# Performance work log

Measured on AMD Instinct MI355X. Metric: run time of the kernel, lower is better.

The kernel has to match this reference:

```python
import jax, jax.numpy as jnp
import numpy as np

TAU = 0.1
B, F_IN, D, K, C = 128, 1000, 512, 10, 5


def setup_inputs() -> dict:
    key = jax.random.key(0)
    ks = jax.random.split(key, 12)
    s = 0.05
    feats = jax.random.normal(ks[0], (B, F_IN), jnp.float32)
    W_adapt = jax.random.normal(ks[1], (F_IN, D), jnp.float32) * s
    b_adapt = jnp.zeros((D,), jnp.float32)
    W_ch = jax.random.normal(ks[2], (C, D, D), jnp.float32) * s   # 5 per-channel Linear(D,D)
    b_ch = jnp.zeros((C, D), jnp.float32)
    W_gate = jax.random.normal(ks[3], (C, D), jnp.float32) * s    # 5 gate Linear(D,1)
    b_gate = jnp.zeros((C,), jnp.float32)
    W_mlp = jax.random.normal(ks[4], (D, K), jnp.float32) * s
    b_mlp = jnp.zeros((K,), jnp.float32)
    T = 1000
    u = jax.random.uniform(ks[5], (B, C, T, 2), jnp.float32, 1e-10, 1.0)
    gumbel = -jnp.log(-jnp.log(u))                                 # Gumbel(0,1) noise, one draw per sample/time
    return {"feats": feats, "W_adapt": W_adapt, "b_adapt": b_adapt,
            "W_ch": W_ch, "b_ch": b_ch, "W_gate": W_gate, "b_gate": b_gate,
            "W_mlp": W_mlp, "b_mlp": b_mlp, "gumbel": gumbel, "repeat_num": T}


def reference(feats, W_adapt, b_adapt, W_ch, b_ch, W_gate, b_gate, W_mlp, b_mlp, gumbel, repeat_num):
    # backbone_output_adapter: Linear(1000, D) + ReLU
    r_b = jax.nn.relu(feats @ W_adapt + b_adapt)                   # [B, D]
    # 5 subjective channels: Linear(D, D) + ReLU each (vectorized over channel axis c)
    h = jax.nn.relu(jnp.einsum('bd,cde->bce', r_b, W_ch) + b_ch)   # [B, C, D]
    # gates: Linear(D, 1) + Sigmoid per channel -> p_t_ [B, C, 1]
    p = jax.nn.sigmoid(jnp.einsum('bcd,cd->bc', h, W_gate) + b_gate)  # [B, C]
    p_t = p[:, :, None]                                            # [B, C, 1]
    # train path: logits = [1-p, p]; repeat_num independent gumbel-softmax draws, vectorized over T
    logits = jnp.stack([1.0 - p, p], axis=-1)                      # [B, C, 2]
    y = jax.nn.softmax((logits[:, :, None, :] + gumbel) / TAU, axis=-1)  # [B, C, T, 2]
    g_t = y[..., 1]                                                # [B, C, T]
    # gate softmax over channel dim, then gated channel mixing
    v_t = jax.nn.softmax(g_t, axis=1)                              # [B, C, T]
    r_g = jnp.einsum('bcd,bct->bdt', h, v_t)                       # [B, D, T]  (256 MB, memory-bound)
    # mlp per time step: Linear(D, K) + ReLU + Softmax(dim=1 over classes)
    logits_s = jax.nn.relu(jnp.einsum('bdt,dk->btk', r_g, W_mlp) + b_mlp)
    r_s = jax.nn.softmax(logits_s, axis=-1)                        # [B, T, K]
    r_s = jnp.transpose(r_s, (1, 0, 2))                            # [T, B, K] == list of T [B,K] outputs
    return (r_s, g_t, p_t)
```

## Files before the change

### kernel.cpp

```cpp
#include <hip/hip_runtime.h>
#include <hip/hip_bf16.h>
#include <math.h>


__global__ __launch_bounds__(256) void kA(const float* __restrict__ feats,
                                          const float* __restrict__ W_adapt,
                                          float* __restrict__ pA) {
    int b0 = blockIdx.x * 4;
    int s  = blockIdx.y;
    int k0 = s * 100;
    int e  = threadIdx.x;
    float acc[4][2] = {};
    #pragma unroll 2
    for (int k = 0; k < 100; ++k) {
        const float* w = &W_adapt[(k0 + k) * 512 + e];
        float w0 = w[0], w1 = w[256];
        #pragma unroll
        for (int j = 0; j < 4; ++j) {
            float f = feats[(b0 + j) * 1000 + k0 + k];
            acc[j][0] = fmaf(f, w0, acc[j][0]);
            acc[j][1] = fmaf(f, w1, acc[j][1]);
        }
    }
    #pragma unroll
    for (int j = 0; j < 4; ++j) {
        pA[(s * 128 + b0 + j) * 512 + e]       = acc[j][0];
        pA[(s * 128 + b0 + j) * 512 + e + 256] = acc[j][1];
    }
}

__global__ __launch_bounds__(256) void kRA(const float* __restrict__ pA,
                                           const float* __restrict__ b_adapt,
                                           float* __restrict__ r_b) {
    int i = blockIdx.x * 256 + threadIdx.x;
    float acc = b_adapt[i & 511];
    #pragma unroll
    for (int s = 0; s < 10; ++s) acc += pA[s * 65536 + i];
    r_b[i] = fmaxf(acc, 0.f);
}

__global__ __launch_bounds__(256) void kB(const float* __restrict__ r_b,
                                          const float* __restrict__ W_ch,
                                          float* __restrict__ pB) {
    int bt = blockIdx.x >> 1, eh = blockIdx.x & 1;
    int s  = blockIdx.y;
    int c  = blockIdx.z;
    int e  = eh * 256 + threadIdx.x;
    int b0 = bt * 8, d0 = s * 128;
    const float* wb = &W_ch[((size_t)c * 512 + d0) * 512 + e];
    const float* rb = &r_b[b0 * 512 + d0];
    float acc[8] = {};
    #pragma unroll 4
    for (int d = 0; d < 128; ++d) {
        float w = wb[d * 512];
        #pragma unroll
        for (int j = 0; j < 8; ++j)
            acc[j] = fmaf(rb[j * 512 + d], w, acc[j]);
    }
    #pragma unroll
    for (int j = 0; j < 8; ++j)
        pB[((s * 5 + c) * 128 + b0 + j) * 512 + e] = acc[j];
}

__global__ __launch_bounds__(256) void kG(const float* __restrict__ pB,
                                          const float* __restrict__ b_ch,
                                          const float* __restrict__ W_gate,
                                          const float* __restrict__ W_mlp,
                                          const float* __restrict__ b_gate,
                                          float* __restrict__ p,
                                          float* __restrict__ M,
                                          float* __restrict__ out_pt) {
    int wv = threadIdx.x >> 6, lane = threadIdx.x & 63;
    int pair = blockIdx.x * 4 + wv;
    int b = pair / 5, c = pair % 5;
    float gs = 0.f, am[10] = {};
    #pragma unroll
    for (int i = 0; i < 8; ++i) {
        int e = i * 64 + lane;
        float hs = b_ch[c * 512 + e];
        #pragma unroll
        for (int s = 0; s < 4; ++s) hs += pB[((s * 5 + c) * 128 + b) * 512 + e];
        float h = fmaxf(hs, 0.f);
        gs = fmaf(h, W_gate[c * 512 + e], gs);
        const float* wm = &W_mlp[e * 10];
        #pragma unroll
        for (int k = 0; k < 10; ++k) am[k] = fmaf(h, wm[k], am[k]);
    }
    #pragma unroll
    for (int off = 32; off; off >>= 1) {
        gs += __shfl_xor(gs, off);
        #pragma unroll
        for (int k = 0; k < 10; ++k) am[k] += __shfl_xor(am[k], off);
    }
    if (lane == 0) {
        float pv = 1.f / (1.f + __expf(-(gs + b_gate[c])));
        p[b * 5 + c] = pv;
        out_pt[b * 5 + c] = pv;
        #pragma unroll
        for (int k = 0; k < 10; ++k) M[(b * 5 + c) * 10 + k] = am[k];
    }
}

__global__ __launch_bounds__(256) void kC(const float* __restrict__ gumbel,
                                          const float* __restrict__ p,
                                          const float* __restrict__ M,
                                          const float* __restrict__ b_mlp,
                                          float* __restrict__ out_rs,
                                          float* __restrict__ out_gt) {
    int t = blockIdx.x * 256 + threadIdx.x;
    int b = blockIdx.y;
    if (t >= 1000) return;
    float ex[5], ssum = 0.f;
    #pragma unroll
    for (int c = 0; c < 5; ++c) {
        float2 gu = *(const float2*)&gumbel[(size_t)(((b * 5 + c) * 1000) + t) * 2];
        float pp  = p[b * 5 + c];
        float arg = (2.f * pp - 1.f + gu.y - gu.x) * 10.0f;
        float gt  = 1.f / (1.f + __expf(-arg));
        out_gt[(b * 5 + c) * 1000 + t] = gt;
        float e = __expf(gt);
        ex[c] = e; ssum += e;
    }
    float inv = 1.f / ssum;
    float lg[10];
    #pragma unroll
    for (int k = 0; k < 10; ++k) lg[k] = b_mlp[k];
    #pragma unroll
    for (int c = 0; c < 5; ++c) {
        float v = ex[c] * inv;
        const float* m = &M[(b * 5 + c) * 10];
        #pragma unroll
        for (int k = 0; k < 10; ++k) lg[k] = fmaf(v, m[k], lg[k]);
    }
    float mx = 0.f;
    #pragma unroll
    for (int k = 0; k < 10; ++k) { lg[k] = fmaxf(lg[k], 0.f); mx = fmaxf(mx, lg[k]); }
    float se = 0.f;
    #pragma unroll
    for (int k = 0; k < 10; ++k) { lg[k] = __expf(lg[k] - mx); se += lg[k]; }
    float invs = 1.f / se;
    float2 outv[5];
    #pragma unroll
    for (int k = 0; k < 10; ++k) ((float*)outv)[k] = lg[k] * invs;
    float2* dst = (float2*)&out_rs[(size_t)t * 1280 + b * 10];
    #pragma unroll
    for (int j = 0; j < 5; ++j) dst[j] = outv[j];
}

extern "C" void kernel_launch(void* const* d_in, const int* in_sizes, int n_in,
                              void* d_out, int out_size, void* d_ws, size_t ws_size,
                              hipStream_t stream) {
    const float* feats   = (const float*)d_in[0];
    const float* W_adapt = (const float*)d_in[1];
    const float* b_adapt = (const float*)d_in[2];
    const float* W_ch    = (const float*)d_in[3];
    const float* b_ch    = (const float*)d_in[4];
    const float* W_gate  = (const float*)d_in[5];
    const float* b_gate  = (const float*)d_in[6];
    const float* W_mlp   = (const float*)d_in[7];
    const float* b_mlp   = (const float*)d_in[8];
    const float* gumbel  = (const float*)d_in[9];

    float* out    = (float*)d_out;
    float* out_rs = out;
    float* out_gt = out + 1280000;
    float* out_pt = out + 1920000;

    float* ws  = (float*)d_ws;
    float* pA  = ws;
    float* r_b = pA + 655360;
    float* pB  = r_b + 65536;
    float* p   = pB + 1310720;
    float* M   = p + 640;

    kA <<<dim3(32, 10),   256, 0, stream>>>(feats, W_adapt, pA);
    kRA<<<256,            256, 0, stream>>>(pA, b_adapt, r_b);
    kB <<<dim3(32, 4, 5), 256, 0, stream>>>(r_b, W_ch, pB);
    kG <<<160,            256, 0, stream>>>(pB, b_ch, W_gate, W_mlp, b_gate, p, M, out_pt);
    kC <<<dim3(4, 128),   256, 0, stream>>>(gumbel, p, M, b_mlp, out_rs, out_gt);
}
```

Before: 51.01 us.

## Fuse split-K reduction into channel GEMM and gate stage into output kernel

```diff
diff --git a/kernel.cpp b/kernel.cpp
--- a/kernel.cpp
+++ b/kernel.cpp
@@ -29,93 +29,111 @@
     }
 }
 
-__global__ __launch_bounds__(256) void kRA(const float* __restrict__ pA,
+__global__ __launch_bounds__(256) void kBR(const float* __restrict__ pA,
                                            const float* __restrict__ b_adapt,
-                                           float* __restrict__ r_b) {
-    int i = blockIdx.x * 256 + threadIdx.x;
-    float acc = b_adapt[i & 511];
-    #pragma unroll
-    for (int s = 0; s < 10; ++s) acc += pA[s * 65536 + i];
-    r_b[i] = fmaxf(acc, 0.f);
-}
-
-__global__ __launch_bounds__(256) void kB(const float* __restrict__ r_b,
-                                          const float* __restrict__ W_ch,
-                                          float* __restrict__ pB) {
+                                           const float* __restrict__ W_ch,
+                                           float* __restrict__ pB) {
+    __shared__ float lds_rb[1024];
     int bt = blockIdx.x >> 1, eh = blockIdx.x & 1;
     int s  = blockIdx.y;
     int c  = blockIdx.z;
-    int e  = eh * 256 + threadIdx.x;
+    int tid = threadIdx.x;
+    int e  = eh * 256 + tid;
     int b0 = bt * 8, d0 = s * 128;
+
+    #pragma unroll
+    for (int i = 0; i < 4; ++i) {
+        int idx = i * 256 + tid;
+        int j = idx >> 7, d = idx & 127;
+        float g = b_adapt[d0 + d];
+        #pragma unroll
+        for (int sp = 0; sp < 10; ++sp)
+            g += pA[sp * 65536 + (b0 + j) * 512 + d0 + d];
+        lds_rb[idx] = fmaxf(g, 0.f);
+    }
+    __syncthreads();
+
     const float* wb = &W_ch[((size_t)c * 512 + d0) * 512 + e];
-    const float* rb = &r_b[b0 * 512 + d0];
     float acc[8] = {};
     #pragma unroll 4
     for (int d = 0; d < 128; ++d) {
         float w = wb[d * 512];
         #pragma unroll
         for (int j = 0; j < 8; ++j)
-            acc[j] = fmaf(rb[j * 512 + d], w, acc[j]);
+            acc[j] = fmaf(lds_rb[j * 128 + d], w, acc[j]);
     }
     #pragma unroll
     for (int j = 0; j < 8; ++j)
         pB[((s * 5 + c) * 128 + b0 + j) * 512 + e] = acc[j];
 }
 
-__global__ __launch_bounds__(256) void kG(const float* __restrict__ pB,
-                                          const float* __restrict__ b_ch,
-                                          const float* __restrict__ W_gate,
-                                          const float* __restrict__ W_mlp,
-                                          const float* __restrict__ b_gate,
-                                          float* __restrict__ p,
-                                          float* __restrict__ M,
-                                          float* __restrict__ out_pt) {
-    int wv = threadIdx.x >> 6, lane = threadIdx.x & 63;
-    int pair = blockIdx.x * 4 + wv;
-    int b = pair / 5, c = pair % 5;
-    float gs = 0.f, am[10] = {};
+__global__ __launch_bounds__(256) void kCM(const float* __restrict__ pB,
+                                           const float* __restrict__ b_ch,
+                                           const float* __restrict__ W_gate,
+                                           const float* __restrict__ W_mlp,
+                                           const float* __restrict__ b_gate,
+                                           const float* __restrict__ b_mlp,
+                                           const float* __restrict__ gumbel,
+                                           float* __restrict__ out_rs,
+                                           float* __restrict__ out_gt,
+                                           float* __restrict__ out_pt) {
+    __shared__ float red[5][12];
+    int tid = threadIdx.x;
+    int wv = tid >> 6, lane = tid & 63;
+    int b = blockIdx.y;
+
     #pragma unroll
-    for (int i = 0; i < 8; ++i) {
-        int e = i * 64 + lane;
-        float hs = b_ch[c * 512 + e];
+    for (int ci = 0; ci < 2; ++ci) {
+        int c = wv + ci * 4;
+        if (c <= 4) {
+            float gs = 0.f, am[10] = {};
+            #pragma unroll
+            for (int i = 0; i < 8; ++i) {
+                int e = i * 64 + lane;
+                float hs = b_ch[c * 512 + e];
+                #pragma unroll
+                for (int sp = 0; sp < 4; ++sp)
+                    hs += pB[((sp * 5 + c) * 128 + b) * 512 + e];
+                float h = fmaxf(hs, 0.f);
+                gs = fmaf(h, W_gate[c * 512 + e], gs);
+                const float* wm = &W_mlp[e * 10];
+                #pragma unroll
+                for (int k = 0; k < 10; ++k) am[k] = fmaf(h, wm[k], am[k]);
+            }
+            #pragma unroll
+            for (int off = 32; off; off >>= 1) {
+                gs += __shfl_xor(gs, off);
+                #pragma unroll
+                for (int k = 0; k < 10; ++k) am[k] += __shfl_xor(am[k], off);
+            }
+            if (lane == 0) {
+                red[c][0] = gs;
+                #pragma unroll
+                for (int k = 0; k < 10; ++k) red[c][1 + k] = am[k];
+            }
+        }
+    }
+    __syncthreads();
+
+    float pv[5], Mv[5][10];
+    #pragma unroll
+    for (int c = 0; c < 5; ++c) {
+        pv[c] = 1.f / (1.f + __expf(-(red[c][0] + b_gate[c])));
         #pragma unroll
-        for (int s = 0; s < 4; ++s) hs += pB[((s * 5 + c) * 128 + b) * 512 + e];
-        float h = fmaxf(hs, 0.f);
-        gs = fmaf(h, W_gate[c * 512 + e], gs);
-        const float* wm = &W_mlp[e * 10];
+        for (int k = 0; k < 10; ++k) Mv[c][k] = red[c][1 + k];
+    }
+    if (blockIdx.x == 0 && tid == 0) {
         #pragma unroll
-        for (int k = 0; k < 10; ++k) am[k] = fmaf(h, wm[k], am[k]);
+        for (int c = 0; c < 5; ++c) out_pt[b * 5 + c] = pv[c];
     }
-    #pragma unroll
-    for (int off = 32; off; off >>= 1) {
-        gs += __shfl_xor(gs, off);
-        #pragma unroll
-        for (int k = 0; k < 10; ++k) am[k] += __shfl_xor(am[k], off);
-    }
-    if (lane == 0) {
-        float pv = 1.f / (1.f + __expf(-(gs + b_gate[c])));
-        p[b * 5 + c] = pv;
-        out_pt[b * 5 + c] = pv;
-        #pragma unroll
-        for (int k = 0; k < 10; ++k) M[(b * 5 + c) * 10 + k] = am[k];
-    }
-}
 
-__global__ __launch_bounds__(256) void kC(const float* __restrict__ gumbel,
-                                          const float* __restrict__ p,
-                                          const float* __restrict__ M,
-                                          const float* __restrict__ b_mlp,
-                                          float* __restrict__ out_rs,
-                                          float* __restrict__ out_gt) {
-    int t = blockIdx.x * 256 + threadIdx.x;
-    int b = blockIdx.y;
+    int t = blockIdx.x * 256 + tid;
     if (t >= 1000) return;
     float ex[5], ssum = 0.f;
     #pragma unroll
     for (int c = 0; c < 5; ++c) {
         float2 gu = *(const float2*)&gumbel[(size_t)(((b * 5 + c) * 1000) + t) * 2];
-        float pp  = p[b * 5 + c];
-        float arg = (2.f * pp - 1.f + gu.y - gu.x) * 10.0f;
+        float arg = (2.f * pv[c] - 1.f + gu.y - gu.x) * 10.0f;
         float gt  = 1.f / (1.f + __expf(-arg));
         out_gt[(b * 5 + c) * 1000 + t] = gt;
         float e = __expf(gt);
@@ -128,9 +146,8 @@
     #pragma unroll
     for (int c = 0; c < 5; ++c) {
         float v = ex[c] * inv;
-        const float* m = &M[(b * 5 + c) * 10];
         #pragma unroll
-        for (int k = 0; k < 10; ++k) lg[k] = fmaf(v, m[k], lg[k]);
+        for (int k = 0; k < 10; ++k) lg[k] = fmaf(v, Mv[c][k], lg[k]);
     }
     float mx = 0.f;
     #pragma unroll
@@ -166,16 +183,12 @@
     float* out_gt = out + 1280000;
     float* out_pt = out + 1920000;
 
-    float* ws  = (float*)d_ws;
-    float* pA  = ws;
-    float* r_b = pA + 655360;
-    float* pB  = r_b + 65536;
-    float* p   = pB + 1310720;
-    float* M   = p + 640;
+    float* ws = (float*)d_ws;
+    float* pA = ws;
+    float* pB = pA + 655360;
 
     kA <<<dim3(32, 10),   256, 0, stream>>>(feats, W_adapt, pA);
-    kRA<<<256,            256, 0, stream>>>(pA, b_adapt, r_b);
-    kB <<<dim3(32, 4, 5), 256, 0, stream>>>(r_b, W_ch, pB);
-    kG <<<160,            256, 0, stream>>>(pB, b_ch, W_gate, W_mlp, b_gate, p, M, out_pt);
-    kC <<<dim3(4, 128),   256, 0, stream>>>(gumbel, p, M, b_mlp, out_rs, out_gt);
+    kBR<<<dim3(32, 4, 5), 256, 0, stream>>>(pA, b_adapt, W_ch, pB);
+    kCM<<<dim3(4, 128),   256, 0, stream>>>(pB, b_ch, W_gate, W_mlp, b_gate,
+                                            b_mlp, gumbel, out_rs, out_gt, out_pt);
 }
```

Result: slower. 56.76 us (+11.3%).

## Vectorize weight loads, reduce channel split-K with atomics, stage params in LDS

Applied to the files above, without the earlier changes.

```diff
diff --git a/kernel.cpp b/kernel.cpp
--- a/kernel.cpp
+++ b/kernel.cpp
@@ -9,61 +9,76 @@
     int b0 = blockIdx.x * 4;
     int s  = blockIdx.y;
     int k0 = s * 100;
-    int e  = threadIdx.x;
-    float acc[4][2] = {};
+    int e2 = threadIdx.x * 2;
+    float2 acc[4] = {};
     #pragma unroll 2
     for (int k = 0; k < 100; ++k) {
-        const float* w = &W_adapt[(k0 + k) * 512 + e];
-        float w0 = w[0], w1 = w[256];
+        float2 w = *(const float2*)&W_adapt[(k0 + k) * 512 + e2];
         #pragma unroll
         for (int j = 0; j < 4; ++j) {
             float f = feats[(b0 + j) * 1000 + k0 + k];
-            acc[j][0] = fmaf(f, w0, acc[j][0]);
-            acc[j][1] = fmaf(f, w1, acc[j][1]);
+            acc[j].x = fmaf(f, w.x, acc[j].x);
+            acc[j].y = fmaf(f, w.y, acc[j].y);
         }
     }
     #pragma unroll
-    for (int j = 0; j < 4; ++j) {
-        pA[(s * 128 + b0 + j) * 512 + e]       = acc[j][0];
-        pA[(s * 128 + b0 + j) * 512 + e + 256] = acc[j][1];
-    }
+    for (int j = 0; j < 4; ++j)
+        *(float2*)&pA[(s * 128 + b0 + j) * 512 + e2] = acc[j];
 }
 
 __global__ __launch_bounds__(256) void kRA(const float* __restrict__ pA,
                                            const float* __restrict__ b_adapt,
-                                           float* __restrict__ r_b) {
+                                           const float* __restrict__ b_ch,
+                                           float* __restrict__ r_b,
+                                           float* __restrict__ hT) {
     int i = blockIdx.x * 256 + threadIdx.x;
-    float acc = b_adapt[i & 511];
+    int e = i & 511;
+    float acc = b_adapt[e];
     #pragma unroll
     for (int s = 0; s < 10; ++s) acc += pA[s * 65536 + i];
     r_b[i] = fmaxf(acc, 0.f);
+    #pragma unroll
+    for (int c = 0; c < 5; ++c) hT[c * 65536 + i] = b_ch[c * 512 + e];
 }
 
 __global__ __launch_bounds__(256) void kB(const float* __restrict__ r_b,
                                           const float* __restrict__ W_ch,
-                                          float* __restrict__ pB) {
-    int bt = blockIdx.x >> 1, eh = blockIdx.x & 1;
-    int s  = blockIdx.y;
+                                          float* __restrict__ hT) {
+    __shared__ float rbs[8 * 128];
+    int b0 = blockIdx.x * 8;
+    int d0 = blockIdx.y * 128;
     int c  = blockIdx.z;
-    int e  = eh * 256 + threadIdx.x;
-    int b0 = bt * 8, d0 = s * 128;
-    const float* wb = &W_ch[((size_t)c * 512 + d0) * 512 + e];
-    const float* rb = &r_b[b0 * 512 + d0];
-    float acc[8] = {};
+    int tid = threadIdx.x;
+
+    #pragma unroll
+    for (int it = 0; it < 4; ++it) {
+        int idx = it * 256 + tid;
+        rbs[idx] = r_b[(b0 + (idx >> 7)) * 512 + d0 + (idx & 127)];
+    }
+    __syncthreads();
+
+    int e2 = tid * 2;
+    const float* wb = &W_ch[((size_t)(c * 512 + d0)) * 512 + e2];
+    float2 acc[8] = {};
     #pragma unroll 4
     for (int d = 0; d < 128; ++d) {
-        float w = wb[d * 512];
+        float2 w = *(const float2*)&wb[(size_t)d * 512];
         #pragma unroll
-        for (int j = 0; j < 8; ++j)
-            acc[j] = fmaf(rb[j * 512 + d], w, acc[j]);
+        for (int j = 0; j < 8; ++j) {
+            float r = rbs[j * 128 + d];
+            acc[j].x = fmaf(r, w.x, acc[j].x);
+            acc[j].y = fmaf(r, w.y, acc[j].y);
+        }
     }
     #pragma unroll
-    for (int j = 0; j < 8; ++j)
-        pB[((s * 5 + c) * 128 + b0 + j) * 512 + e] = acc[j];
+    for (int j = 0; j < 8; ++j) {
+        float* dst = &hT[(c * 128 + b0 + j) * 512 + e2];
+        atomicAdd(dst,     acc[j].x);
+        atomicAdd(dst + 1, acc[j].y);
+    }
 }
 
-__global__ __launch_bounds__(256) void kG(const float* __restrict__ pB,
-                                          const float* __restrict__ b_ch,
+__global__ __launch_bounds__(256) void kG(const float* __restrict__ hT,
                                           const float* __restrict__ W_gate,
                                           const float* __restrict__ W_mlp,
                                           const float* __restrict__ b_gate,
@@ -77,10 +92,7 @@
     #pragma unroll
     for (int i = 0; i < 8; ++i) {
         int e = i * 64 + lane;
-        float hs = b_ch[c * 512 + e];
-        #pragma unroll
-        for (int s = 0; s < 4; ++s) hs += pB[((s * 5 + c) * 128 + b) * 512 + e];
-        float h = fmaxf(hs, 0.f);
+        float h = fmaxf(hT[(c * 128 + b) * 512 + e], 0.f);
         gs = fmaf(h, W_gate[c * 512 + e], gs);
         const float* wm = &W_mlp[e * 10];
         #pragma unroll
@@ -101,21 +113,27 @@
     }
 }
 
-__global__ __launch_bounds__(256) void kC(const float* __restrict__ gumbel,
-                                          const float* __restrict__ p,
+__global__ __launch_bounds__(256) void kC(const float* __restrict__ p,
                                           const float* __restrict__ M,
                                           const float* __restrict__ b_mlp,
+                                          const float* __restrict__ gumbel,
                                           float* __restrict__ out_rs,
                                           float* __restrict__ out_gt) {
-    int t = blockIdx.x * 256 + threadIdx.x;
+    __shared__ float spv[5];
+    __shared__ float sM[50];
+    int tid = threadIdx.x;
     int b = blockIdx.y;
+    if (tid < 50) sM[tid] = M[b * 50 + tid];
+    if (tid < 5)  spv[tid] = p[b * 5 + tid];
+    __syncthreads();
+
+    int t = blockIdx.x * 256 + tid;
     if (t >= 1000) return;
     float ex[5], ssum = 0.f;
     #pragma unroll
     for (int c = 0; c < 5; ++c) {
         float2 gu = *(const float2*)&gumbel[(size_t)(((b * 5 + c) * 1000) + t) * 2];
-        float pp  = p[b * 5 + c];
-        float arg = (2.f * pp - 1.f + gu.y - gu.x) * 10.0f;
+        float arg = (2.f * spv[c] - 1.f + gu.y - gu.x) * 10.0f;
         float gt  = 1.f / (1.f + __expf(-arg));
         out_gt[(b * 5 + c) * 1000 + t] = gt;
         float e = __expf(gt);
@@ -128,9 +146,8 @@
     #pragma unroll
     for (int c = 0; c < 5; ++c) {
         float v = ex[c] * inv;
-        const float* m = &M[(b * 5 + c) * 10];
         #pragma unroll
-        for (int k = 0; k < 10; ++k) lg[k] = fmaf(v, m[k], lg[k]);
+        for (int k = 0; k < 10; ++k) lg[k] = fmaf(v, sM[c * 10 + k], lg[k]);
     }
     float mx = 0.f;
     #pragma unroll
@@ -169,13 +186,13 @@
     float* ws  = (float*)d_ws;
     float* pA  = ws;
     float* r_b = pA + 655360;
-    float* pB  = r_b + 65536;
-    float* p   = pB + 1310720;
+    float* hT  = r_b + 65536;
+    float* p   = hT + 327680;
     float* M   = p + 640;
 
     kA <<<dim3(32, 10),   256, 0, stream>>>(feats, W_adapt, pA);
-    kRA<<<256,            256, 0, stream>>>(pA, b_adapt, r_b);
-    kB <<<dim3(32, 4, 5), 256, 0, stream>>>(r_b, W_ch, pB);
-    kG <<<160,            256, 0, stream>>>(pB, b_ch, W_gate, W_mlp, b_gate, p, M, out_pt);
-    kC <<<dim3(4, 128),   256, 0, stream>>>(gumbel, p, M, b_mlp, out_rs, out_gt);
+    kRA<<<256,            256, 0, stream>>>(pA, b_adapt, b_ch, r_b, hT);
+    kB <<<dim3(16, 4, 5), 256, 0, stream>>>(r_b, W_ch, hT);
+    kG <<<160,            256, 0, stream>>>(hT, W_gate, W_mlp, b_gate, p, M, out_pt);
+    kC <<<dim3(4, 128),   256, 0, stream>>>(p, M, b_mlp, gumbel, out_rs, out_gt);
 }
```

New measurement: 56.69 us. 1.11x slower.
